# Performance work log

Hardware: AMD Instinct MI355X
Metric: run time of the kernel (lower is better)

## Reference

```python
import jax, jax.numpy as jnp
import numpy as np

N = 50176          # total nodes (128 alternating ligand/protein segments x 392 nodes)
SEGS = 128         # 2*B -> B = 64 complexes
PER = 392
E_BI = N * 4       # covalent-bond graph, avg degree 4
E_KNN = N * 16     # knn spatial graph, avg degree 16
F_IN = 64
D = 128            # f_bond = f_spatial
F_GATHER = 128
N_BOND_STEPS = 2
N_SPATIAL_STEPS = 2

def _lin(k, fi, fo):
    return jax.random.normal(k, (fi, fo), jnp.float32) / np.sqrt(fi)

def setup_inputs():
    ks = iter(jax.random.split(jax.random.key(0), 64))
    inp = {}
    inp["feat"] = jax.random.normal(next(ks), (N, F_IN), jnp.float32)
    inp["bi_src"] = jax.random.randint(next(ks), (E_BI,), 0, N)
    inp["bi_dst"] = jax.random.randint(next(ks), (E_BI,), 0, N)
    inp["bi_etype"] = jax.random.randint(next(ks), (E_BI,), 0, 5)
    inp["knn_src"] = jax.random.randint(next(ks), (E_KNN,), 0, N)
    inp["knn_dst"] = jax.random.randint(next(ks), (E_KNN,), 0, N)
    inp["knn_etype"] = jax.random.randint(next(ks), (E_KNN,), 0, 9)
    inp["batch_num_nodes"] = jnp.full((SEGS,), PER, jnp.int32)
    def gg(prefix, in_f, n_et):
        inp[prefix + "_W"] = jax.random.normal(next(ks), (n_et, D, D), jnp.float32) / np.sqrt(D)
        inp[prefix + "_b"] = jnp.zeros((n_et, D), jnp.float32)
        inp[prefix + "_wih"] = _lin(next(ks), D, 3 * D)
        inp[prefix + "_whh"] = _lin(next(ks), D, 3 * D)
        inp[prefix + "_bih"] = jnp.zeros((3 * D,), jnp.float32)
        inp[prefix + "_bhh"] = jnp.zeros((3 * D,), jnp.float32)
        inp[prefix + "_iw"] = _lin(next(ks), in_f + D, F_GATHER)
        inp[prefix + "_ib"] = jnp.zeros((F_GATHER,), jnp.float32)
        inp[prefix + "_jw"] = _lin(next(ks), D, F_GATHER)
        inp[prefix + "_jb"] = jnp.zeros((F_GATHER,), jnp.float32)
    gg("s1", F_IN, 5)
    gg("s2", F_GATHER, 9)
    inp["s3_w0"] = _lin(next(ks), F_GATHER, 256)
    inp["s3_b0"] = jnp.zeros((256,), jnp.float32)
    inp["s3_w1"] = _lin(next(ks), 256, 128)
    inp["s3_b1"] = jnp.zeros((128,), jnp.float32)
    inp["s3_wo"] = _lin(next(ks), 128, 1)
    inp["s3_bo"] = jnp.zeros((1,), jnp.float32)
    return inp

def _ggc(feat, src, dst, etype, W, b, wih, whh, bih, bhh, iw, ib, jw, jb, n_steps):
    n_nodes = feat.shape[0]
    n_et, d, _ = W.shape
    h = jnp.pad(feat, ((0, 0), (0, d - feat.shape[1])))  # zero_pad to out_feats
    def step(h, _):
        h_src = h[src]  # [E, d] gather
        m = jnp.zeros((src.shape[0], d), h.dtype)
        for i in range(n_et):  # per-edge-type linear, masked by one-hot edge type
            m = m + jnp.where((etype == i)[:, None], h_src @ W[i] + b[i], 0.0)
        a = jax.ops.segment_sum(m, dst, num_segments=n_nodes)  # scatter-sum (fn.sum)
        ir, iz, i_n = jnp.split(a @ wih + bih, 3, axis=-1)     # GRUCell, gate order r,z,n
        hr, hz, hn = jnp.split(h @ whh + bhh, 3, axis=-1)
        r = jax.nn.sigmoid(ir + hr)
        z = jax.nn.sigmoid(iz + hz)
        n = jnp.tanh(i_n + r * hn)
        return (1.0 - z) * n + z * h, None
    h, _ = jax.lax.scan(step, h, None, length=n_steps)
    # dropout is identity in eval mode
    return jax.nn.sigmoid(jnp.concatenate([h, feat], axis=1) @ iw + ib) * (h @ jw + jb)

def reference(feat, bi_src, bi_dst, bi_etype, knn_src, knn_dst, knn_etype, batch_num_nodes,
              s1_W, s1_b, s1_wih, s1_whh, s1_bih, s1_bhh, s1_iw, s1_ib, s1_jw, s1_jb,
              s2_W, s2_b, s2_wih, s2_whh, s2_bih, s2_bhh, s2_iw, s2_ib, s2_jw, s2_jb,
              s3_w0, s3_b0, s3_w1, s3_b1, s3_wo, s3_bo):
    h = _ggc(feat, bi_src, bi_dst, bi_etype, s1_W, s1_b, s1_wih, s1_whh, s1_bih, s1_bhh,
             s1_iw, s1_ib, s1_jw, s1_jb, N_BOND_STEPS)
    h = _ggc(h, knn_src, knn_dst, knn_etype, s2_W, s2_b, s2_wih, s2_whh, s2_bih, s2_bhh,
             s2_iw, s2_ib, s2_jw, s2_jb, N_SPATIAL_STEPS)
    segs = batch_num_nodes.shape[0]
    seg_id = jnp.repeat(jnp.arange(segs), batch_num_nodes, total_repeat_length=h.shape[0])
    pooled = jax.ops.segment_sum(h, seg_id, num_segments=segs)[0::2]  # ligand (even) segments
    x = jax.nn.relu(pooled @ s3_w0 + s3_b0)
    x = jax.nn.relu(x @ s3_w1 + s3_b1)
    return x @ s3_wo + s3_bo
```

## Files before the change

### kernel.cpp

```cpp
#include <hip/hip_runtime.h>
#include <hip/hip_bf16.h>

#define N_NODES 50176
#define PER 392
#define E_BI (N_NODES * 4)
#define E_KNN (N_NODES * 16)
#define E_TOT (E_BI + E_KNN)
#define KN_BI (N_NODES * 5)
#define KN_TOT (N_NODES * 14)
#define AH_S 416
#define AH_U 208

typedef __attribute__((ext_vector_type(8))) short short8;
typedef __attribute__((ext_vector_type(4))) float float4v;
typedef unsigned int uint;
typedef unsigned short ushort;

__device__ __forceinline__ float sigmoidf_(float x) { return 1.f / (1.f + __expf(-x)); }
__device__ __forceinline__ ushort f2bu(float x) {
    __hip_bfloat16 t = __float2bfloat16(x);
    return *reinterpret_cast<ushort*>(&t);
}
__device__ __forceinline__ float blo(uint u) { return __uint_as_float(u << 16); }
__device__ __forceinline__ float bhi(uint u) { return __uint_as_float(u & 0xFFFF0000u); }

template<int NET>
__global__ __launch_bounds__(256) void msg_kernel(
    const uint* __restrict__ hb,
    const int* __restrict__ indptr,
    const int* __restrict__ elist,
    const ushort* __restrict__ Bfrag,
    ushort* __restrict__ aout)
{
    __shared__ ushort As[4][32][40];
    const int tid = threadIdx.x;
    const int bm = blockIdx.x * 32;
    const int wave = tid >> 6, lane = tid & 63;
    const int quad = lane >> 4, lrow = lane & 15;
    const int wr = wave & 1, wc = wave >> 1;
    const int r = tid >> 3;
    const int oct = tid & 7;
    const int v = bm + r;

    uint* AsU = (uint*)As;

    float4v acc[4] = {};

    for (int et = 0; et < NET; et++) {
        const int beg = indptr[v * NET + et], end = indptr[v * NET + et + 1];
        float av[16];
#pragma unroll
        for (int i = 0; i < 16; i++) av[i] = 0.f;

        for (int j = beg; j < end; j++) {
            int src = elist[j];
            const uint4* hp = (const uint4*)(hb + (size_t)src * 64 + oct * 8);
            uint4 u0 = hp[0];
            uint4 u1 = hp[1];
            av[0] += blo(u0.x); av[1] += bhi(u0.x);
            av[2] += blo(u0.y); av[3] += bhi(u0.y);
            av[4] += blo(u0.z); av[5] += bhi(u0.z);
            av[6] += blo(u0.w); av[7] += bhi(u0.w);
            av[8]  += blo(u1.x); av[9]  += bhi(u1.x);
            av[10] += blo(u1.y); av[11] += bhi(u1.y);
            av[12] += blo(u1.z); av[13] += bhi(u1.z);
            av[14] += blo(u1.w); av[15] += bhi(u1.w);
        }

        __syncthreads();
        {
            int base = ((oct >> 1) * 32 + r) * 20 + (oct & 1) * 8;
#pragma unroll
            for (int u = 0; u < 8; u++)
                AsU[base + u] = (uint)f2bu(av[2 * u]) | ((uint)f2bu(av[2 * u + 1]) << 16);
        }
        __syncthreads();

#pragma unroll
        for (int ch = 0; ch < 4; ch++) {
            short8 af = *(const short8*)&As[ch][wr * 16 + lrow][quad * 8];
            const ushort* bp = Bfrag + ((size_t)(((et * 4 + ch) * 2 + wc) * 4) << 9) + lane * 8;
#pragma unroll
            for (int j = 0; j < 4; j++) {
                short8 bfr = *(const short8*)(bp + j * 512);
                acc[j] = __builtin_amdgcn_mfma_f32_16x16x32_bf16(af, bfr, acc[j], 0, 0, 0);
            }
        }
    }

#pragma unroll
    for (int j = 0; j < 4; j++) {
        int col = wc * 64 + j * 16 + lrow;
#pragma unroll
        for (int rr = 0; rr < 4; rr++) {
            size_t row = (size_t)(bm + wr * 16 + quad * 4 + rr);
            aout[row * AH_S + col] = f2bu(acc[j][rr]);
        }
    }
}

__global__ __launch_bounds__(256) void gru_gemm_kernel(
    const ushort* __restrict__ A,
    const ushort* __restrict__ Bt,
    const float* __restrict__ bias,
    float* __restrict__ h,
    ushort* __restrict__ ahOut, ushort* __restrict__ hbS)
{
    __shared__ ushort As[128 * 32];
    __shared__ ushort Bs[128 * 32];
    const int tid = threadIdx.x;
    const int bm = blockIdx.x * 128;
    const int bn = blockIdx.y * 128;
    const int wave = tid >> 6, lane = tid & 63;
    const int quad = lane >> 4, lrow = lane & 15;
    const int wr = wave & 1, wc = wave >> 1;

    float4v acc[4][4] = {};

    for (int k0 = 0; k0 < 288; k0 += 32) {
        __syncthreads();
#pragma unroll
        for (int p = 0; p < 2; p++) {
            int lin = p * 256 + tid;
            int r = lin >> 2;
            int kc = (lin & 3) * 8;
            *(short8*)&As[r * 32 + kc] = *(const short8*)(A + (size_t)(bm + r) * AH_S + k0 + kc);
            *(short8*)&Bs[r * 32 + kc] = *(const short8*)(Bt + (size_t)(bn + r) * 288 + k0 + kc);
        }
        __syncthreads();
        short8 af[4], bfr[4];
#pragma unroll
        for (int i = 0; i < 4; i++)
            af[i] = *(const short8*)&As[(wr * 64 + i * 16 + lrow) * 32 + quad * 8];
#pragma unroll
        for (int j = 0; j < 4; j++)
            bfr[j] = *(const short8*)&Bs[(wc * 64 + j * 16 + lrow) * 32 + quad * 8];
#pragma unroll
        for (int i = 0; i < 4; i++)
#pragma unroll
            for (int j = 0; j < 4; j++)
                acc[i][j] = __builtin_amdgcn_mfma_f32_16x16x32_bf16(af[i], bfr[j], acc[i][j], 0, 0, 0);
    }

    const int ch = (bn >> 7) * 32 + wc * 16 + lrow;
    const float b0 = bias[bn + wc * 64 + lrow];
    const float b1 = bias[bn + wc * 64 + 16 + lrow];
    const float b2 = bias[bn + wc * 64 + 32 + lrow];
    const float b3 = bias[bn + wc * 64 + 48 + lrow];
#pragma unroll
    for (int i = 0; i < 4; i++) {
#pragma unroll
        for (int r = 0; r < 4; r++) {
            size_t row = (size_t)(bm + wr * 64 + i * 16 + quad * 4 + r);
            float rr = sigmoidf_(acc[i][0][r] + b0);
            float zz = sigmoidf_(acc[i][1][r] + b1);
            float nn = tanhf(acc[i][2][r] + b2 + rr * (acc[i][3][r] + b3));
            float hold = h[row * 128 + ch];
            float hnew = (1.f - zz) * nn + zz * hold;
            h[row * 128 + ch] = hnew;
            ushort hu = f2bu(hnew);
            ahOut[row * AH_S + 128 + ch] = hu;
            hbS[row * 128 + ch] = hu;
        }
    }
}

__global__ __launch_bounds__(256) void ro_gemm_kernel(
    const ushort* __restrict__ A,
    const ushort* __restrict__ Bt,
    const float* __restrict__ bias,
    float* __restrict__ rout, ushort* __restrict__ rb)
{
    __shared__ ushort As[128 * 32];
    __shared__ ushort Bs[128 * 32];
    const int tid = threadIdx.x;
    const int bm = blockIdx.x * 128;
    const int bn = blockIdx.y * 128;
    const int wave = tid >> 6, lane = tid & 63;
    const int quad = lane >> 4, lrow = lane & 15;
    const int wr = wave & 1, wc = wave >> 1;

    float4v acc[4][4] = {};

    for (int k0 = 0; k0 < 288; k0 += 32) {
        __syncthreads();
#pragma unroll
        for (int p = 0; p < 2; p++) {
            int lin = p * 256 + tid;
            int r = lin >> 2;
            int kc = (lin & 3) * 8;
            *(short8*)&As[r * 32 + kc] = *(const short8*)(A + (size_t)(bm + r) * AH_S + k0 + kc);
            *(short8*)&Bs[r * 32 + kc] = *(const short8*)(Bt + (size_t)(bn + r) * 288 + k0 + kc);
        }
        __syncthreads();
        short8 af[4], bfr[4];
#pragma unroll
        for (int i = 0; i < 4; i++)
            af[i] = *(const short8*)&As[(wr * 64 + i * 16 + lrow) * 32 + quad * 8];
#pragma unroll
        for (int j = 0; j < 4; j++)
            bfr[j] = *(const short8*)&Bs[(wc * 64 + j * 16 + lrow) * 32 + quad * 8];
#pragma unroll
        for (int i = 0; i < 4; i++)
#pragma unroll
            for (int j = 0; j < 4; j++)
                acc[i][j] = __builtin_amdgcn_mfma_f32_16x16x32_bf16(af[i], bfr[j], acc[i][j], 0, 0, 0);
    }

    const int c0 = (bn >> 7) * 64 + wc * 32 + lrow;
    const int c1 = c0 + 16;
    const float bu0 = bias[bn + wc * 64 + lrow];
    const float bv0 = bias[bn + wc * 64 + 16 + lrow];
    const float bu1 = bias[bn + wc * 64 + 32 + lrow];
    const float bv1 = bias[bn + wc * 64 + 48 + lrow];
#pragma unroll
    for (int i = 0; i < 4; i++) {
#pragma unroll
        for (int r = 0; r < 4; r++) {
            size_t row = (size_t)(bm + wr * 64 + i * 16 + quad * 4 + r);
            float o0 = sigmoidf_(acc[i][0][r] + bu0) * (acc[i][1][r] + bv0);
            float o1 = sigmoidf_(acc[i][2][r] + bu1) * (acc[i][3][r] + bv1);
            if (rout) { rout[row * 128 + c0] = o0; rout[row * 128 + c1] = o1; }
            if (rb)   { rb[row * 128 + c0] = f2bu(o0); rb[row * 128 + c1] = f2bu(o1); }
        }
    }
}

__global__ __launch_bounds__(256) void gemm_kernel(
    const float* __restrict__ A, int lda,
    const float* __restrict__ B, int ldb,
    const float* __restrict__ bias,
    float* __restrict__ C, int ldc,
    int K, int act)
{
    __shared__ float As[32][68];
    __shared__ float Bs[32][68];
    const int tid = threadIdx.x;
    const int bm = blockIdx.x * 64;
    const int bn = blockIdx.y * 64;
    const int tm = (tid & 15) * 4;
    const int tn = (tid >> 4) * 4;
    float acc[4][4] = {};

    for (int k0 = 0; k0 < K; k0 += 32) {
#pragma unroll
        for (int p = 0; p < 2; p++) {
            int lin = p * 256 + tid;
            int ar = lin >> 3;
            int ac = (lin & 7) << 2;
            float4 av = *(const float4*)(A + (size_t)(bm + ar) * lda + (k0 + ac));
            As[ac + 0][ar] = av.x;
            As[ac + 1][ar] = av.y;
            As[ac + 2][ar] = av.z;
            As[ac + 3][ar] = av.w;
            int br = lin >> 4;
            int bc = (lin & 15) << 2;
            *(float4*)&Bs[br][bc] = *(const float4*)(B + (size_t)(k0 + br) * ldb + (bn + bc));
        }
        __syncthreads();
#pragma unroll
        for (int k = 0; k < 32; k++) {
            float4 a4 = *(const float4*)&As[k][tm];
            float4 b4 = *(const float4*)&Bs[k][tn];
            float av[4] = {a4.x, a4.y, a4.z, a4.w};
            float bv[4] = {b4.x, b4.y, b4.z, b4.w};
#pragma unroll
            for (int i = 0; i < 4; i++)
#pragma unroll
                for (int j = 0; j < 4; j++)
                    acc[i][j] += av[i] * bv[j];
        }
        __syncthreads();
    }
#pragma unroll
    for (int i = 0; i < 4; i++) {
        size_t row = (size_t)(bm + tm + i);
#pragma unroll
        for (int j = 0; j < 4; j++) {
            int col = bn + tn + j;
            float val = acc[i][j] + (bias ? bias[col] : 0.f);
            if (act == 1) val = fmaxf(val, 0.f);
            C[row * ldc + col] = val;
        }
    }
}

__global__ void prep_bfrag_kernel(const float* __restrict__ W, __hip_bfloat16* __restrict__ Bf,
                                  int net)
{
    int idx = blockIdx.x * blockDim.x + threadIdx.x;
    int m = idx & 7;
    int lane = (idx >> 3) & 63;
    int f = idx >> 9;
    int j = f & 3; f >>= 2;
    int wc = f & 1; f >>= 1;
    int ch = f & 3;
    int et = f >> 2;
    int quad = lane >> 4, lrow = lane & 15;
    int k = ch * 32 + quad * 8 + m;
    int c = wc * 64 + j * 16 + lrow;
    Bf[idx] = __float2bfloat16(W[et * 16384 + k * 128 + c]);
}

__global__ void prep_gru_kernel(const float* __restrict__ wih, const float* __restrict__ whh,
                                const float* __restrict__ bih, const float* __restrict__ bhh,
                                const float* __restrict__ b, int net,
                                __hip_bfloat16* __restrict__ Bt, float* __restrict__ bias)
{
    int idx = blockIdx.x * blockDim.x + threadIdx.x;
    int p = idx / 288;
    int k = idx - p * 288;
    int g = (p >> 4) & 3;
    int c = (p >> 7) * 32 + ((p >> 6) & 1) * 16 + (p & 15);
    float val = 0.f;
    if (k < 128) {
        if (g == 0)      val = wih[k * 384 + c];
        else if (g == 1) val = wih[k * 384 + 128 + c];
        else if (g == 2) val = wih[k * 384 + 256 + c];
    } else if (k < 256) {
        int kk = k - 128;
        if (g == 0)      val = whh[kk * 384 + c];
        else if (g == 1) val = whh[kk * 384 + 128 + c];
        else if (g == 3) val = whh[kk * 384 + 256 + c];
    } else {
        int j = k - 256;
        if (j < net && g < 3) {
            int col = g * 128 + c;
            float s = 0.f;
            for (int kk = 0; kk < 128; kk++) s += b[j * 128 + kk] * wih[kk * 384 + col];
            val = s;
        }
    }
    Bt[idx] = __float2bfloat16(val);
    if (k == 0) {
        float bv;
        if (g == 0)      bv = bih[c] + bhh[c];
        else if (g == 1) bv = bih[128 + c] + bhh[128 + c];
        else if (g == 2) bv = bih[256 + c];
        else             bv = bhh[256 + c];
        bias[p] = bv;
    }
}

__global__ void prep_ro_kernel(const float* __restrict__ iw, const float* __restrict__ jw,
                               const float* __restrict__ ib, const float* __restrict__ jb,
                               int Fin, __hip_bfloat16* __restrict__ Bt,
                               float* __restrict__ bias)
{
    int idx = blockIdx.x * blockDim.x + threadIdx.x;
    int p = idx / 288;
    int k = idx - p * 288;
    int j = (p >> 4) & 3;
    int s = j & 1;
    int c = ((p >> 7) & 1) * 64 + ((p >> 6) & 1) * 32 + (j >> 1) * 16 + (p & 15);
    float val = 0.f;
    if (k < 128) {
        val = s ? jw[k * 128 + c] : iw[k * 128 + c];
    } else if (k >= 160) {
        int kf = k - 160;
        if (kf < Fin && s == 0) val = iw[(128 + kf) * 128 + c];
    }
    Bt[idx] = __float2bfloat16(val);
    if (k == 0) bias[p] = s ? jb[c] : ib[c];
}

__global__ void hist2_kernel(const int* __restrict__ bd, const int* __restrict__ be,
                             const int* __restrict__ kd, const int* __restrict__ ke,
                             int* __restrict__ counts)
{
    int e = blockIdx.x * blockDim.x + threadIdx.x;
    if (e >= E_TOT) return;
    if (e < E_BI) atomicAdd(&counts[bd[e] * 5 + be[e]], 1);
    else { int i = e - E_BI; atomicAdd(&counts[KN_BI + kd[i] * 9 + ke[i]], 1); }
}

__global__ void scan1_kernel(const int* __restrict__ counts, int* __restrict__ local_ex,
                             int* __restrict__ partial)
{
    __shared__ int s[256];
    int t = threadIdx.x;
    int i = blockIdx.x * 256 + t;
    int v = counts[i];
    s[t] = v;
    __syncthreads();
    for (int off = 1; off < 256; off <<= 1) {
        int x = 0;
        if (t >= off) x = s[t - off];
        __syncthreads();
        if (t >= off) s[t] += x;
        __syncthreads();
    }
    local_ex[i] = s[t] - v;
    if (t == 255) partial[blockIdx.x] = s[255];
}

__global__ void scan2b_kernel(int* __restrict__ partial, int nb, int* __restrict__ last, int E)
{
    __shared__ int s[256];
    int t = threadIdx.x;
    int loc[11];
    int sum = 0;
#pragma unroll
    for (int q = 0; q < 11; q++) {
        int idx = t * 11 + q;
        int v = (idx < nb) ? partial[idx] : 0;
        loc[q] = sum; sum += v;
    }
    s[t] = sum;
    __syncthreads();
    for (int off = 1; off < 256; off <<= 1) {
        int x = 0;
        if (t >= off) x = s[t - off];
        __syncthreads();
        if (t >= off) s[t] += x;
        __syncthreads();
    }
    int excl = s[t] - sum;
#pragma unroll
    for (int q = 0; q < 11; q++) {
        int idx = t * 11 + q;
        if (idx < nb) partial[idx] = excl + loc[q];
    }
    if (t == 0) *last = E;
}

__global__ void scan3c_kernel(int* __restrict__ indptr, const int* __restrict__ partial,
                              int* __restrict__ cursor)
{
    int i = blockIdx.x * 256 + threadIdx.x;
    int v = indptr[i] + partial[blockIdx.x];
    indptr[i] = v;
    cursor[i] = v;
}

__global__ void fill2_kernel(const int* __restrict__ bs, const int* __restrict__ bd,
                             const int* __restrict__ be,
                             const int* __restrict__ ks, const int* __restrict__ kd,
                             const int* __restrict__ ke,
                             int* __restrict__ cursor, int* __restrict__ elist)
{
    int e = blockIdx.x * blockDim.x + threadIdx.x;
    if (e >= E_TOT) return;
    if (e < E_BI) {
        int pos = atomicAdd(&cursor[bd[e] * 5 + be[e]], 1);
        elist[pos] = bs[e];
    } else {
        int i = e - E_BI;
        int pos = atomicAdd(&cursor[KN_BI + kd[i] * 9 + ke[i]], 1);
        elist[pos] = ks[i];
    }
}

__global__ void cnt_kernel(const int* __restrict__ indptr, int net,
                           ushort* __restrict__ ahA, ushort* __restrict__ ahB)
{
    int idx = blockIdx.x * blockDim.x + threadIdx.x;
    int v = idx >> 5;
    int j = idx & 31;
    float cv = 0.f;
    if (j < net) cv = (float)(indptr[v * net + j + 1] - indptr[v * net + j]);
    ushort u = f2bu(cv);
    ahA[(size_t)v * AH_S + 256 + j] = u;
    ahB[(size_t)v * AH_S + 256 + j] = u;
}

__global__ void pad_kernel(const float* __restrict__ fsrc, const ushort* __restrict__ bsrc,
                           float* __restrict__ h, uint* __restrict__ ahA,
                           uint* __restrict__ ahB, uint* __restrict__ hb, int Fin)
{
    int idx = blockIdx.x * blockDim.x + threadIdx.x;
    int v = idx >> 5;
    int c = (idx & 31) * 4;
    float4 val = make_float4(0.f, 0.f, 0.f, 0.f);
    if (bsrc) {
        uint2 u = *(const uint2*)(bsrc + (size_t)v * Fin + c);
        val.x = blo(u.x); val.y = bhi(u.x);
        val.z = blo(u.y); val.w = bhi(u.y);
    } else if (c < Fin) {
        val = *(const float4*)(fsrc + (size_t)v * Fin + c);
    }
    *(float4*)(h + (size_t)v * 128 + c) = val;
    uint2 pk;
    pk.x = (uint)f2bu(val.x) | ((uint)f2bu(val.y) << 16);
    pk.y = (uint)f2bu(val.z) | ((uint)f2bu(val.w) << 16);
    *(uint2*)(ahA + (size_t)v * AH_U + 64 + c / 2) = pk;
    *(uint2*)(ahA + (size_t)v * AH_U + 144 + c / 2) = pk;
    *(uint2*)(ahB + (size_t)v * AH_U + 144 + c / 2) = pk;
    *(uint2*)(hb + (size_t)v * 64 + c / 2) = pk;
}

__global__ void pool_kernel(const float* __restrict__ r2, float* __restrict__ pooled)
{
    int s = blockIdx.x;
    int c = threadIdx.x;
    const float* base = r2 + (size_t)(2 * s) * PER * 128;
    float acc = 0.f;
    for (int i = 0; i < PER; i++) acc += base[(size_t)i * 128 + c];
    pooled[s * 128 + c] = acc;
}

__global__ void out_kernel(const float* __restrict__ x2, const float* __restrict__ wo,
                           const float* __restrict__ bo, float* __restrict__ out)
{
    int row = blockIdx.x;
    int t = threadIdx.x;
    float s = x2[row * 128 + t] * wo[t] + x2[row * 128 + 64 + t] * wo[64 + t];
#pragma unroll
    for (int off = 32; off; off >>= 1) s += __shfl_down(s, off);
    if (t == 0) out[row] = s + bo[0];
}

struct GGParams {
    const float *W, *b, *wih, *whh, *bih, *bhh, *iw, *ib, *jw, *jb;
};

struct WsPtrs {
    float* h;
    __hip_bfloat16 *ah0, *ah1;
    float* G;
    uint* hb;
    __hip_bfloat16* r1b;
    __hip_bfloat16 *bfragB, *gruB, *roB;
    float *gruBias, *roBias;
    int *indptr, *cursor, *partial, *elist;
    float *pooled, *x1, *x2;
};

template<int NET>
static void run_stage(hipStream_t st, const float* featF, const __hip_bfloat16* featB, int Fin,
                      const GGParams& p, const WsPtrs& w, const int* indptr_slice,
                      float* rout, __hip_bfloat16* rout_b)
{
    const int N = N_NODES;
    ushort* ahA = (ushort*)w.ah0;
    ushort* ahB = (ushort*)w.ah1;
    ushort* hbS = (ushort*)w.hb;

    prep_bfrag_kernel<<<(NET * 16384) / 256, 256, 0, st>>>(p.W, w.bfragB, NET);
    prep_gru_kernel<<<(512 * 288) / 256, 256, 0, st>>>(p.wih, p.whh, p.bih, p.bhh, p.b, NET,
                                                       w.gruB, w.gruBias);
    prep_ro_kernel<<<(256 * 288) / 256, 256, 0, st>>>(p.iw, p.jw, p.ib, p.jb, Fin,
                                                      w.roB, w.roBias);

    cnt_kernel<<<(N * 32) / 256, 256, 0, st>>>(indptr_slice, NET, ahA, ahB);
    pad_kernel<<<(N * 32) / 256, 256, 0, st>>>(featF, (const ushort*)featB, w.h,
                                               (uint*)ahA, (uint*)ahB, w.hb, Fin);

    ushort* ahIn = ahA;
    ushort* ahOut = ahB;
    for (int step = 0; step < 2; step++) {
        msg_kernel<NET><<<N / 32, 256, 0, st>>>(w.hb, indptr_slice, w.elist,
                                                (ushort*)w.bfragB, ahIn);
        dim3 g(N / 128, 4);
        gru_gemm_kernel<<<g, 256, 0, st>>>(ahIn, (ushort*)w.gruB, w.gruBias, w.h, ahOut, hbS);
        ushort* t = ahIn; ahIn = ahOut; ahOut = t;
    }
    dim3 gr(N / 128, 2);
    ro_gemm_kernel<<<gr, 256, 0, st>>>(ahIn + 128, (ushort*)w.roB, w.roBias,
                                       rout, (ushort*)rout_b);
}

extern "C" void kernel_launch(void* const* d_in, const int* in_sizes, int n_in,
                              void* d_out, int out_size, void* d_ws, size_t ws_size,
                              hipStream_t stream)
{
    const float* feat    = (const float*)d_in[0];
    const int*   bi_src  = (const int*)d_in[1];
    const int*   bi_dst  = (const int*)d_in[2];
    const int*   bi_et   = (const int*)d_in[3];
    const int*   knn_src = (const int*)d_in[4];
    const int*   knn_dst = (const int*)d_in[5];
    const int*   knn_et  = (const int*)d_in[6];

    GGParams s1 { (const float*)d_in[8],  (const float*)d_in[9],  (const float*)d_in[10],
                  (const float*)d_in[11], (const float*)d_in[12], (const float*)d_in[13],
                  (const float*)d_in[14], (const float*)d_in[15], (const float*)d_in[16],
                  (const float*)d_in[17] };
    GGParams s2 { (const float*)d_in[18], (const float*)d_in[19], (const float*)d_in[20],
                  (const float*)d_in[21], (const float*)d_in[22], (const float*)d_in[23],
                  (const float*)d_in[24], (const float*)d_in[25], (const float*)d_in[26],
                  (const float*)d_in[27] };
    const float* w0 = (const float*)d_in[28];
    const float* b0 = (const float*)d_in[29];
    const float* w1 = (const float*)d_in[30];
    const float* b1 = (const float*)d_in[31];
    const float* wo = (const float*)d_in[32];
    const float* bo = (const float*)d_in[33];

    const int N = N_NODES;
    const size_t n128 = (size_t)N * 128;

    float* ws = (float*)d_ws;
    WsPtrs w;
    size_t off = 0;
    w.h      = ws + off;                       off += n128;
    w.ah0    = (__hip_bfloat16*)(ws + off);    off += (size_t)N * 208;
    w.ah1    = (__hip_bfloat16*)(ws + off);    off += (size_t)N * 208;
    w.G      = ws + off;                       off += 2 * n128;
    w.hb     = (uint*)(w.G + n128);
    w.r1b    = (__hip_bfloat16*)(ws + off);    off += n128 / 2;
    w.bfragB = (__hip_bfloat16*)(ws + off);    off += 9 * 16384 / 2;
    w.gruB   = (__hip_bfloat16*)(ws + off);    off += 512 * 288 / 2;
    w.roB    = (__hip_bfloat16*)(ws + off);    off += 256 * 288 / 2;
    w.gruBias = ws + off;                      off += 512;
    w.roBias  = ws + off;                      off += 256;
    w.indptr  = (int*)(ws + off);              off += KN_TOT + 8;
    w.cursor  = (int*)(ws + off);              off += KN_TOT;
    w.partial = (int*)(ws + off);              off += 4096;
    w.elist   = (int*)(ws + off);              off += E_TOT;
    w.pooled  = ws + off;                      off += 64 * 128;
    w.x1      = ws + off;                      off += 64 * 256;
    w.x2      = ws + off;                      off += 64 * 128;

    hipMemsetAsync(w.cursor, 0, KN_TOT * sizeof(int), stream);
    hist2_kernel<<<(E_TOT + 255) / 256, 256, 0, stream>>>(bi_dst, bi_et, knn_dst, knn_et, w.cursor);
    scan1_kernel<<<KN_TOT / 256, 256, 0, stream>>>(w.cursor, w.indptr, w.partial);
    scan2b_kernel<<<1, 256, 0, stream>>>(w.partial, KN_TOT / 256, w.indptr + KN_TOT, E_TOT);
    scan3c_kernel<<<KN_TOT / 256, 256, 0, stream>>>(w.indptr, w.partial, w.cursor);
    fill2_kernel<<<(E_TOT + 255) / 256, 256, 0, stream>>>(bi_src, bi_dst, bi_et,
                                                          knn_src, knn_dst, knn_et,
                                                          w.cursor, w.elist);

    run_stage<5>(stream, feat, nullptr, 64, s1, w, w.indptr, nullptr, w.r1b);
    float* rout2 = w.G;
    run_stage<9>(stream, nullptr, w.r1b, 128, s2, w, w.indptr + KN_BI, rout2, nullptr);

    pool_kernel<<<64, 128, 0, stream>>>(rout2, w.pooled);
    {
        dim3 g1(1, 4);
        gemm_kernel<<<g1, 256, 0, stream>>>(w.pooled, 128, w0, 256, b0, w.x1, 256, 128, 1);
        dim3 g2(1, 2);
        gemm_kernel<<<g2, 256, 0, stream>>>(w.x1, 256, w1, 128, b1, w.x2, 128, 256, 1);
    }
    out_kernel<<<64, 64, 0, stream>>>(w.x2, wo, bo, (float*)d_out);
}
```

Measured before the change: 777.5 us.

## Split msg_kernel edge gather across two thread groups and fuse pad/cnt kernels

The message kernel now launches 512 threads per block. Each node's edge list is split between two 8-lane groups by parity, and their partial sums are combined with a cross-lane shuffle before the shared-memory store. The MFMA work is spread over 8 waves, each covering 32 output columns, which doubles the memory-level parallelism of the irregular gather at the cost of an extra shuffle reduction and half the threads idling during the store. Separately, the count and padding kernels are merged into one launch to save a kernel launch and an indptr-related pass.

```diff
diff --git a/kernel.cpp b/kernel.cpp
--- a/kernel.cpp
+++ b/kernel.cpp
@@ -25,7 +25,7 @@
 __device__ __forceinline__ float bhi(uint u) { return __uint_as_float(u & 0xFFFF0000u); }
 
 template<int NET>
-__global__ __launch_bounds__(256) void msg_kernel(
+__global__ __launch_bounds__(512) void msg_kernel(
     const uint* __restrict__ hb,
     const int* __restrict__ indptr,
     const int* __restrict__ elist,
@@ -37,14 +37,15 @@
     const int bm = blockIdx.x * 32;
     const int wave = tid >> 6, lane = tid & 63;
     const int quad = lane >> 4, lrow = lane & 15;
-    const int wr = wave & 1, wc = wave >> 1;
-    const int r = tid >> 3;
+    const int wr = wave & 1, wcol = wave >> 1;
+    const int r = tid >> 4;
+    const int par = (tid >> 3) & 1;
     const int oct = tid & 7;
     const int v = bm + r;
 
     uint* AsU = (uint*)As;
 
-    float4v acc[4] = {};
+    float4v acc[2] = {};
 
     for (int et = 0; et < NET; et++) {
         const int beg = indptr[v * NET + et], end = indptr[v * NET + et + 1];
@@ -52,7 +53,7 @@
 #pragma unroll
         for (int i = 0; i < 16; i++) av[i] = 0.f;
 
-        for (int j = beg; j < end; j++) {
+        for (int j = beg + par; j < end; j += 2) {
             int src = elist[j];
             const uint4* hp = (const uint4*)(hb + (size_t)src * 64 + oct * 8);
             uint4 u0 = hp[0];
@@ -66,9 +67,11 @@
             av[12] += blo(u1.z); av[13] += bhi(u1.z);
             av[14] += blo(u1.w); av[15] += bhi(u1.w);
         }
-
-        __syncthreads();
-        {
+#pragma unroll
+        for (int i = 0; i < 16; i++) av[i] += __shfl_xor(av[i], 8);
+
+        __syncthreads();
+        if (par == 0) {
             int base = ((oct >> 1) * 32 + r) * 20 + (oct & 1) * 8;
 #pragma unroll
             for (int u = 0; u < 8; u++)
@@ -79,9 +82,11 @@
 #pragma unroll
         for (int ch = 0; ch < 4; ch++) {
             short8 af = *(const short8*)&As[ch][wr * 16 + lrow][quad * 8];
-            const ushort* bp = Bfrag + ((size_t)(((et * 4 + ch) * 2 + wc) * 4) << 9) + lane * 8;
-#pragma unroll
-            for (int j = 0; j < 4; j++) {
+            const ushort* bp = Bfrag +
+                ((size_t)((((et * 4 + ch) * 2 + (wcol >> 1)) * 4) + (wcol & 1) * 2) << 9)
+                + lane * 8;
+#pragma unroll
+            for (int j = 0; j < 2; j++) {
                 short8 bfr = *(const short8*)(bp + j * 512);
                 acc[j] = __builtin_amdgcn_mfma_f32_16x16x32_bf16(af, bfr, acc[j], 0, 0, 0);
             }
@@ -89,8 +94,8 @@
     }
 
 #pragma unroll
-    for (int j = 0; j < 4; j++) {
-        int col = wc * 64 + j * 16 + lrow;
+    for (int j = 0; j < 2; j++) {
+        int col = wcol * 32 + j * 16 + lrow;
 #pragma unroll
         for (int rr = 0; rr < 4; rr++) {
             size_t row = (size_t)(bm + wr * 16 + quad * 4 + rr);
@@ -451,26 +456,15 @@
     }
 }
 
-__global__ void cnt_kernel(const int* __restrict__ indptr, int net,
-                           ushort* __restrict__ ahA, ushort* __restrict__ ahB)
+__global__ void pad_cnt_kernel(const float* __restrict__ fsrc, const ushort* __restrict__ bsrc,
+                               const int* __restrict__ indptr, int net,
+                               float* __restrict__ h, uint* __restrict__ ahA,
+                               uint* __restrict__ ahB, uint* __restrict__ hb, int Fin)
 {
     int idx = blockIdx.x * blockDim.x + threadIdx.x;
     int v = idx >> 5;
     int j = idx & 31;
-    float cv = 0.f;
-    if (j < net) cv = (float)(indptr[v * net + j + 1] - indptr[v * net + j]);
-    ushort u = f2bu(cv);
-    ahA[(size_t)v * AH_S + 256 + j] = u;
-    ahB[(size_t)v * AH_S + 256 + j] = u;
-}
-
-__global__ void pad_kernel(const float* __restrict__ fsrc, const ushort* __restrict__ bsrc,
-                           float* __restrict__ h, uint* __restrict__ ahA,
-                           uint* __restrict__ ahB, uint* __restrict__ hb, int Fin)
-{
-    int idx = blockIdx.x * blockDim.x + threadIdx.x;
-    int v = idx >> 5;
-    int c = (idx & 31) * 4;
+    int c = j * 4;
     float4 val = make_float4(0.f, 0.f, 0.f, 0.f);
     if (bsrc) {
         uint2 u = *(const uint2*)(bsrc + (size_t)v * Fin + c);
@@ -487,6 +481,11 @@
     *(uint2*)(ahA + (size_t)v * AH_U + 144 + c / 2) = pk;
     *(uint2*)(ahB + (size_t)v * AH_U + 144 + c / 2) = pk;
     *(uint2*)(hb + (size_t)v * 64 + c / 2) = pk;
+    float cv = 0.f;
+    if (j < net) cv = (float)(indptr[v * net + j + 1] - indptr[v * net + j]);
+    ushort u = f2bu(cv);
+    ((ushort*)ahA)[(size_t)v * AH_S + 256 + j] = u;
+    ((ushort*)ahB)[(size_t)v * AH_S + 256 + j] = u;
 }
 
 __global__ void pool_kernel(const float* __restrict__ r2, float* __restrict__ pooled)
@@ -542,14 +541,14 @@
     prep_ro_kernel<<<(256 * 288) / 256, 256, 0, st>>>(p.iw, p.jw, p.ib, p.jb, Fin,
                                                       w.roB, w.roBias);
 
-    cnt_kernel<<<(N * 32) / 256, 256, 0, st>>>(indptr_slice, NET, ahA, ahB);
-    pad_kernel<<<(N * 32) / 256, 256, 0, st>>>(featF, (const ushort*)featB, w.h,
-                                               (uint*)ahA, (uint*)ahB, w.hb, Fin);
+    pad_cnt_kernel<<<(N * 32) / 256, 256, 0, st>>>(featF, (const ushort*)featB,
+                                                   indptr_slice, NET, w.h,
+                                                   (uint*)ahA, (uint*)ahB, w.hb, Fin);
 
     ushort* ahIn = ahA;
     ushort* ahOut = ahB;
     for (int step = 0; step < 2; step++) {
-        msg_kernel<NET><<<N / 32, 256, 0, st>>>(w.hb, indptr_slice, w.elist,
+        msg_kernel<NET><<<N / 32, 512, 0, st>>>(w.hb, indptr_slice, w.elist,
                                                 (ushort*)w.bfragB, ahIn);
         dim3 g(N / 128, 4);
         gru_gemm_kernel<<<g, 256, 0, st>>>(ahIn, (ushort*)w.gruB, w.gruBias, w.h, ahOut, hbS);
```

Result: slower. 801.2 us (+3.0%).

## Drop fp32 hidden state buffer, unroll gather by two, fuse pad and count kernels

Applied to the files above, without the earlier changes.

The fp32 hidden-state array is removed. The GRU kernel now reads the old hidden value from the bf16 copy already held in its A operand and no longer writes fp32 h. The readout writes only bf16, which pool then consumes, and the separate count and pad kernels are merged into one launch. The message gather loop is unrolled by two so two neighbour rows are loaded in flight at once. Together these cut global memory traffic and launch count, at the cost of keeping the recurrent state and final readout in bf16 precision only.

```diff
diff --git a/kernel.cpp b/kernel.cpp
--- a/kernel.cpp
+++ b/kernel.cpp
@@ -52,7 +52,24 @@
 #pragma unroll
         for (int i = 0; i < 16; i++) av[i] = 0.f;
 
-        for (int j = beg; j < end; j++) {
+        int j = beg;
+        for (; j + 2 <= end; j += 2) {
+            int s0 = elist[j];
+            int s1 = elist[j + 1];
+            const uint4* p0 = (const uint4*)(hb + (size_t)s0 * 64 + oct * 8);
+            const uint4* p1 = (const uint4*)(hb + (size_t)s1 * 64 + oct * 8);
+            uint4 a0 = p0[0], a1 = p0[1];
+            uint4 b0 = p1[0], b1 = p1[1];
+            av[0] += blo(a0.x) + blo(b0.x); av[1] += bhi(a0.x) + bhi(b0.x);
+            av[2] += blo(a0.y) + blo(b0.y); av[3] += bhi(a0.y) + bhi(b0.y);
+            av[4] += blo(a0.z) + blo(b0.z); av[5] += bhi(a0.z) + bhi(b0.z);
+            av[6] += blo(a0.w) + blo(b0.w); av[7] += bhi(a0.w) + bhi(b0.w);
+            av[8]  += blo(a1.x) + blo(b1.x); av[9]  += bhi(a1.x) + bhi(b1.x);
+            av[10] += blo(a1.y) + blo(b1.y); av[11] += bhi(a1.y) + bhi(b1.y);
+            av[12] += blo(a1.z) + blo(b1.z); av[13] += bhi(a1.z) + bhi(b1.z);
+            av[14] += blo(a1.w) + blo(b1.w); av[15] += bhi(a1.w) + bhi(b1.w);
+        }
+        if (j < end) {
             int src = elist[j];
             const uint4* hp = (const uint4*)(hb + (size_t)src * 64 + oct * 8);
             uint4 u0 = hp[0];
@@ -81,20 +98,20 @@
             short8 af = *(const short8*)&As[ch][wr * 16 + lrow][quad * 8];
             const ushort* bp = Bfrag + ((size_t)(((et * 4 + ch) * 2 + wc) * 4) << 9) + lane * 8;
 #pragma unroll
-            for (int j = 0; j < 4; j++) {
-                short8 bfr = *(const short8*)(bp + j * 512);
-                acc[j] = __builtin_amdgcn_mfma_f32_16x16x32_bf16(af, bfr, acc[j], 0, 0, 0);
+            for (int j2 = 0; j2 < 4; j2++) {
+                short8 bfr = *(const short8*)(bp + j2 * 512);
+                acc[j2] = __builtin_amdgcn_mfma_f32_16x16x32_bf16(af, bfr, acc[j2], 0, 0, 0);
             }
         }
     }
 
 #pragma unroll
-    for (int j = 0; j < 4; j++) {
-        int col = wc * 64 + j * 16 + lrow;
+    for (int j2 = 0; j2 < 4; j2++) {
+        int col = wc * 64 + j2 * 16 + lrow;
 #pragma unroll
         for (int rr = 0; rr < 4; rr++) {
             size_t row = (size_t)(bm + wr * 16 + quad * 4 + rr);
-            aout[row * AH_S + col] = f2bu(acc[j][rr]);
+            aout[row * AH_S + col] = f2bu(acc[j2][rr]);
         }
     }
 }
@@ -103,7 +120,6 @@
     const ushort* __restrict__ A,
     const ushort* __restrict__ Bt,
     const float* __restrict__ bias,
-    float* __restrict__ h,
     ushort* __restrict__ ahOut, ushort* __restrict__ hbS)
 {
     __shared__ ushort As[128 * 32];
@@ -155,9 +171,8 @@
             float rr = sigmoidf_(acc[i][0][r] + b0);
             float zz = sigmoidf_(acc[i][1][r] + b1);
             float nn = tanhf(acc[i][2][r] + b2 + rr * (acc[i][3][r] + b3));
-            float hold = h[row * 128 + ch];
+            float hold = __uint_as_float(((uint)A[row * AH_S + 128 + ch]) << 16);
             float hnew = (1.f - zz) * nn + zz * hold;
-            h[row * 128 + ch] = hnew;
             ushort hu = f2bu(hnew);
             ahOut[row * AH_S + 128 + ch] = hu;
             hbS[row * 128 + ch] = hu;
@@ -169,7 +184,7 @@
     const ushort* __restrict__ A,
     const ushort* __restrict__ Bt,
     const float* __restrict__ bias,
-    float* __restrict__ rout, ushort* __restrict__ rb)
+    ushort* __restrict__ rb)
 {
     __shared__ ushort As[128 * 32];
     __shared__ ushort Bs[128 * 32];
@@ -220,8 +235,8 @@
             size_t row = (size_t)(bm + wr * 64 + i * 16 + quad * 4 + r);
             float o0 = sigmoidf_(acc[i][0][r] + bu0) * (acc[i][1][r] + bv0);
             float o1 = sigmoidf_(acc[i][2][r] + bu1) * (acc[i][3][r] + bv1);
-            if (rout) { rout[row * 128 + c0] = o0; rout[row * 128 + c1] = o1; }
-            if (rb)   { rb[row * 128 + c0] = f2bu(o0); rb[row * 128 + c1] = f2bu(o1); }
+            rb[row * 128 + c0] = f2bu(o0);
+            rb[row * 128 + c1] = f2bu(o1);
         }
     }
 }
@@ -451,26 +466,15 @@
     }
 }
 
-__global__ void cnt_kernel(const int* __restrict__ indptr, int net,
-                           ushort* __restrict__ ahA, ushort* __restrict__ ahB)
+__global__ void pad_cnt_kernel(const float* __restrict__ fsrc, const ushort* __restrict__ bsrc,
+                               const int* __restrict__ indptr, int net,
+                               uint* __restrict__ ahA, uint* __restrict__ ahB,
+                               uint* __restrict__ hb, int Fin)
 {
     int idx = blockIdx.x * blockDim.x + threadIdx.x;
     int v = idx >> 5;
     int j = idx & 31;
-    float cv = 0.f;
-    if (j < net) cv = (float)(indptr[v * net + j + 1] - indptr[v * net + j]);
-    ushort u = f2bu(cv);
-    ahA[(size_t)v * AH_S + 256 + j] = u;
-    ahB[(size_t)v * AH_S + 256 + j] = u;
-}
-
-__global__ void pad_kernel(const float* __restrict__ fsrc, const ushort* __restrict__ bsrc,
-                           float* __restrict__ h, uint* __restrict__ ahA,
-                           uint* __restrict__ ahB, uint* __restrict__ hb, int Fin)
-{
-    int idx = blockIdx.x * blockDim.x + threadIdx.x;
-    int v = idx >> 5;
-    int c = (idx & 31) * 4;
+    int c = j * 4;
     float4 val = make_float4(0.f, 0.f, 0.f, 0.f);
     if (bsrc) {
         uint2 u = *(const uint2*)(bsrc + (size_t)v * Fin + c);
@@ -479,7 +483,6 @@
     } else if (c < Fin) {
         val = *(const float4*)(fsrc + (size_t)v * Fin + c);
     }
-    *(float4*)(h + (size_t)v * 128 + c) = val;
     uint2 pk;
     pk.x = (uint)f2bu(val.x) | ((uint)f2bu(val.y) << 16);
     pk.y = (uint)f2bu(val.z) | ((uint)f2bu(val.w) << 16);
@@ -487,15 +490,21 @@
     *(uint2*)(ahA + (size_t)v * AH_U + 144 + c / 2) = pk;
     *(uint2*)(ahB + (size_t)v * AH_U + 144 + c / 2) = pk;
     *(uint2*)(hb + (size_t)v * 64 + c / 2) = pk;
-}
-
-__global__ void pool_kernel(const float* __restrict__ r2, float* __restrict__ pooled)
+    float cv = 0.f;
+    if (j < net) cv = (float)(indptr[v * net + j + 1] - indptr[v * net + j]);
+    ushort u = f2bu(cv);
+    ((ushort*)ahA)[(size_t)v * AH_S + 256 + j] = u;
+    ((ushort*)ahB)[(size_t)v * AH_S + 256 + j] = u;
+}
+
+__global__ void pool_kernel(const ushort* __restrict__ r2, float* __restrict__ pooled)
 {
     int s = blockIdx.x;
     int c = threadIdx.x;
-    const float* base = r2 + (size_t)(2 * s) * PER * 128;
+    const ushort* base = r2 + (size_t)(2 * s) * PER * 128;
     float acc = 0.f;
-    for (int i = 0; i < PER; i++) acc += base[(size_t)i * 128 + c];
+    for (int i = 0; i < PER; i++)
+        acc += __uint_as_float(((uint)base[(size_t)i * 128 + c]) << 16);
     pooled[s * 128 + c] = acc;
 }
 
@@ -515,7 +524,6 @@
 };
 
 struct WsPtrs {
-    float* h;
     __hip_bfloat16 *ah0, *ah1;
     float* G;
     uint* hb;
@@ -529,7 +537,7 @@
 template<int NET>
 static void run_stage(hipStream_t st, const float* featF, const __hip_bfloat16* featB, int Fin,
                       const GGParams& p, const WsPtrs& w, const int* indptr_slice,
-                      float* rout, __hip_bfloat16* rout_b)
+                      __hip_bfloat16* rout_b)
 {
     const int N = N_NODES;
     ushort* ahA = (ushort*)w.ah0;
@@ -542,9 +550,9 @@
     prep_ro_kernel<<<(256 * 288) / 256, 256, 0, st>>>(p.iw, p.jw, p.ib, p.jb, Fin,
                                                       w.roB, w.roBias);
 
-    cnt_kernel<<<(N * 32) / 256, 256, 0, st>>>(indptr_slice, NET, ahA, ahB);
-    pad_kernel<<<(N * 32) / 256, 256, 0, st>>>(featF, (const ushort*)featB, w.h,
-                                               (uint*)ahA, (uint*)ahB, w.hb, Fin);
+    pad_cnt_kernel<<<(N * 32) / 256, 256, 0, st>>>(featF, (const ushort*)featB,
+                                                   indptr_slice, NET,
+                                                   (uint*)ahA, (uint*)ahB, w.hb, Fin);
 
     ushort* ahIn = ahA;
     ushort* ahOut = ahB;
@@ -552,12 +560,12 @@
         msg_kernel<NET><<<N / 32, 256, 0, st>>>(w.hb, indptr_slice, w.elist,
                                                 (ushort*)w.bfragB, ahIn);
         dim3 g(N / 128, 4);
-        gru_gemm_kernel<<<g, 256, 0, st>>>(ahIn, (ushort*)w.gruB, w.gruBias, w.h, ahOut, hbS);
+        gru_gemm_kernel<<<g, 256, 0, st>>>(ahIn, (ushort*)w.gruB, w.gruBias, ahOut, hbS);
         ushort* t = ahIn; ahIn = ahOut; ahOut = t;
     }
     dim3 gr(N / 128, 2);
     ro_gemm_kernel<<<gr, 256, 0, st>>>(ahIn + 128, (ushort*)w.roB, w.roBias,
-                                       rout, (ushort*)rout_b);
+                                       (ushort*)rout_b);
 }
 
 extern "C" void kernel_launch(void* const* d_in, const int* in_sizes, int n_in,
@@ -593,7 +601,6 @@
     float* ws = (float*)d_ws;
     WsPtrs w;
     size_t off = 0;
-    w.h      = ws + off;                       off += n128;
     w.ah0    = (__hip_bfloat16*)(ws + off);    off += (size_t)N * 208;
     w.ah1    = (__hip_bfloat16*)(ws + off);    off += (size_t)N * 208;
     w.G      = ws + off;                       off += 2 * n128;
@@ -621,11 +628,11 @@
                                                           knn_src, knn_dst, knn_et,
                                                           w.cursor, w.elist);
 
-    run_stage<5>(stream, feat, nullptr, 64, s1, w, w.indptr, nullptr, w.r1b);
-    float* rout2 = w.G;
-    run_stage<9>(stream, nullptr, w.r1b, 128, s2, w, w.indptr + KN_BI, rout2, nullptr);
-
-    pool_kernel<<<64, 128, 0, stream>>>(rout2, w.pooled);
+    run_stage<5>(stream, feat, nullptr, 64, s1, w, w.indptr, w.r1b);
+    __hip_bfloat16* r2b = (__hip_bfloat16*)w.G;
+    run_stage<9>(stream, nullptr, w.r1b, 128, s2, w, w.indptr + KN_BI, r2b);
+
+    pool_kernel<<<64, 128, 0, stream>>>((const ushort*)r2b, w.pooled);
     {
         dim3 g1(1, 4);
         gemm_kernel<<<g1, 256, 0, stream>>>(w.pooled, 128, w0, 256, b0, w.x1, 256, 128, 1);
```

Result: no change. 768.9 us (-1.1%).
